# Performance work log

Hardware: AMD Instinct MI355X
Metric: run time of the kernel (lower is better)

## Reference

```python
import jax, jax.numpy as jnp
import numpy as np

GRID_SIZE = 5
SPLINE_ORDER = 3
NUM_BASIS = GRID_SIZE + SPLINE_ORDER  # 8


def make_grid():
    # knots: grid_size + 2*spline_order + 1 = 12 points over extended [-1,1]
    h = 2.0 / GRID_SIZE
    return (jnp.arange(-SPLINE_ORDER, GRID_SIZE + SPLINE_ORDER + 1, dtype=jnp.float32) * h - 1.0)[None, :]  # (1, 12)


def b_splines(x, grid):
    # x: (N, in) -> bases: (N, in, NUM_BASIS) via Cox-de Boor recursion
    x = x[..., None]  # (N, in, 1)
    bases = ((x >= grid[:, :-1]) & (x < grid[:, 1:])).astype(x.dtype)
    for p in range(1, SPLINE_ORDER + 1):
        left = (x - grid[:, : -(p + 1)]) / (grid[:, p:-1] - grid[:, : -(p + 1)])
        right = (grid[:, p + 1:] - x) / (grid[:, p + 1:] - grid[:, 1:-p])
        bases = left * bases[..., :-1] + right * bases[..., 1:]
    return bases


def kan_linear(x, base_w, spline_w, scaler, grid):
    # x: (N, in); base_w: (out, in); spline_w: (out, in, G); scaler: (out, in)
    base = jnp.einsum('ni,oi->no', jax.nn.silu(x), base_w)
    bases = b_splines(x, grid)  # (N, in, G)
    spline = jnp.einsum('nig,oig->no', bases, spline_w * scaler[..., None])
    return base + spline


def setup_inputs() -> dict:
    key = jax.random.key(0)
    ks = jax.random.split(key, 7)
    H, L = 768, 2
    hidden = jax.random.normal(ks[0], (32, 512, H), dtype=jnp.float32)
    s = 0.1
    return {
        'hidden': hidden,
        'base_w1': jax.random.normal(ks[1], (H, H), jnp.float32) * s,
        'spline_w1': jax.random.normal(ks[2], (H, H, NUM_BASIS), jnp.float32) * s,
        'scaler1': jax.random.normal(ks[3], (H, H), jnp.float32) * s + 1.0,
        'base_w2': jax.random.normal(ks[4], (L, H), jnp.float32) * s,
        'spline_w2': jax.random.normal(ks[5], (L, H, NUM_BASIS), jnp.float32) * s,
        'scaler2': jax.random.normal(ks[6], (L, H), jnp.float32) * s + 1.0,
    }


def reference(hidden, base_w1, spline_w1, scaler1, base_w2, spline_w2, scaler2):
    grid = make_grid()
    B, S, H = hidden.shape
    x = hidden.reshape(-1, H)  # (N, H)
    x = kan_linear(x, base_w1, spline_w1, scaler1, grid)
    x = jax.nn.gelu(x, approximate=False)  # torch F.gelu default = erf
    out = kan_linear(x, base_w2, spline_w2, scaler2, grid)  # (N, L)
    return out.reshape(B, S, -1).squeeze(-1) if out.shape[-1] == 1 else out.reshape(B, S, -1)
```

## Files before the change

kernel.cpp:

```cpp
#include <hip/hip_runtime.h>
#include <math.h>

#define NROWS 16384
#define H     768
#define KEXP  6912
#define NCHUNK 108
#define NITER 54

typedef __attribute__((ext_vector_type(8))) short  bhalf8;
typedef __attribute__((ext_vector_type(4))) float  floatx4;
typedef __attribute__((ext_vector_type(4))) unsigned int uintx4;

__device__ __forceinline__ unsigned short f2bf(float f) {
    unsigned int u = __float_as_uint(f);
    u = (u + 0x7FFFu + ((u >> 16) & 1u)) >> 16;
    return (unsigned short)u;
}
__device__ __forceinline__ float bf2f(unsigned short h) {
    return __uint_as_float(((unsigned int)h) << 16);
}
__device__ __forceinline__ unsigned int pack2(unsigned short a, unsigned short b) {
    return (unsigned int)a | ((unsigned int)b << 16);
}
__device__ __forceinline__ float silu_f(float x) {
    return x * __builtin_amdgcn_rcpf(1.0f + __expf(-x));
}

__device__ __forceinline__ float gelu_fast(float x) {
    float x3 = x * x * x;
    float y = fmaf(x3, 0.0356774081f, x * 0.7978845608f);
    float e = __expf(2.0f * y);
    float th = 1.0f - 2.0f * __builtin_amdgcn_rcpf(e + 1.0f);
    return 0.5f * x * (1.0f + th);
}

__device__ __forceinline__ void kan_bases(float x, float* __restrict__ b) {
    const float c6 = 0.166666666667f;
    float u  = fmaf(x, 2.5f, 5.5f);
    float fj = floorf(u);
    float t  = u - fj;
    int  j0  = (int)fj;
    float t2 = t * t, t3 = t2 * t;
    float n0 = t3 * c6;
    float n1 = fmaf(t3, -0.5f, fmaf(t2, 0.5f, fmaf(t, 0.5f, c6)));
    float n2 = fmaf(t3, 0.5f, fmaf(t2, -1.0f, 0.666666666667f));
    float omt = 1.0f - t;
    float n3 = omt * omt * omt * c6;
#pragma unroll
    for (int c = 0; c < 8; ++c) {
        int d = j0 - c;
        float v = (d == 0) ? n0 : 0.0f;
        v = (d == 1) ? n1 : v;
        v = (d == 2) ? n2 : v;
        v = (d == 3) ? n3 : v;
        b[c] = v;
    }
}

__global__ __launch_bounds__(256) void prep_expand(
    const float* __restrict__ x, const float* __restrict__ bw,
    const float* __restrict__ sw, const float* __restrict__ sc,
    unsigned short* __restrict__ wp, unsigned short* __restrict__ F)
{
    const int b = blockIdx.x, t = threadIdx.x;
    if (b < 6144) {
        const int e0 = b * 2048 + t;
#pragma unroll
        for (int j = 0; j < 8; ++j) {
            int e = e0 + j * 256;
            int n = e / 768;
            int i = e - n * 768;
            float xv = x[e];
            unsigned short* out = F + (size_t)n * KEXP;
            __builtin_nontemporal_store(f2bf(silu_f(xv)), out + i);
            float bb[8];
            kan_bases(xv, bb);
            uintx4 pk;
            pk.x = pack2(f2bf(bb[0]), f2bf(bb[1]));
            pk.y = pack2(f2bf(bb[2]), f2bf(bb[3]));
            pk.z = pack2(f2bf(bb[4]), f2bf(bb[5]));
            pk.w = pack2(f2bf(bb[6]), f2bf(bb[7]));
            __builtin_nontemporal_store(pk, (uintx4*)(out + H + (size_t)i * 8));
        }
    } else {
        const int n = b - 6144;
        const float* bwr = bw + (size_t)n * H;
        unsigned short* out = wp + (size_t)n * KEXP;
        if (t < 96) {
            const float4* xp = (const float4*)(bwr + t * 8);
            float4 v0 = xp[0], v1 = xp[1];
            uintx4 pk;
            pk.x = pack2(f2bf(v0.x), f2bf(v0.y));
            pk.y = pack2(f2bf(v0.z), f2bf(v0.w));
            pk.z = pack2(f2bf(v1.x), f2bf(v1.y));
            pk.w = pack2(f2bf(v1.z), f2bf(v1.w));
            __builtin_nontemporal_store(pk, (uintx4*)(out + t * 8));
        }
#pragma unroll
        for (int p = 0; p < 3; ++p) {
            int i = t + p * 256;
            float s = sc[(size_t)n * H + i];
            const float4* swp = (const float4*)(sw + ((size_t)n * H + i) * 8);
            float4 w0 = swp[0], w1 = swp[1];
            uintx4 pk;
            pk.x = pack2(f2bf(w0.x * s), f2bf(w0.y * s));
            pk.y = pack2(f2bf(w0.z * s), f2bf(w0.w * s));
            pk.z = pack2(f2bf(w1.x * s), f2bf(w1.y * s));
            pk.w = pack2(f2bf(w1.z * s), f2bf(w1.w * s));
            __builtin_nontemporal_store(pk, (uintx4*)(out + H + (size_t)i * 8));
        }
    }
}


#define AS1 __attribute__((address_space(1)))
#define AS3 __attribute__((address_space(3)))

#define DSR(D, A, O) asm volatile("ds_read_b128 %0, %1 offset:" #O : "=v"(D) : "v"(A) : "memory")
#define LDA0(O) do{ DSR(fA0[0],avA[0],O); DSR(fA0[1],avA[1],O); DSR(fA0[2],avA[2],O); DSR(fA0[3],avA[3],O); \
                    DSR(fA0[4],avA[4],O); DSR(fA0[5],avA[5],O); DSR(fA0[6],avA[6],O); DSR(fA0[7],avA[7],O); }while(0)
#define LDA1(O) do{ DSR(fA1[0],avA[0],O); DSR(fA1[1],avA[1],O); DSR(fA1[2],avA[2],O); DSR(fA1[3],avA[3],O); \
                    DSR(fA1[4],avA[4],O); DSR(fA1[5],avA[5],O); DSR(fA1[6],avA[6],O); DSR(fA1[7],avA[7],O); }while(0)
#define LDB(O)  do{ DSR(fB[0],avB[0],O); DSR(fB[1],avB[1],O); }while(0)

#define MM0(QN) do{ \
    _Pragma("unroll") \
    for (int kk = 0; kk < 2; ++kk) \
        _Pragma("unroll") \
        for (int im = 0; im < 4; ++im) \
            acc0[QN][im] = __builtin_amdgcn_mfma_f32_16x16x32_bf16( \
                fA0[im*2+kk], fB[kk], acc0[QN][im], 0, 0, 0); \
}while(0)
#define MM1(QN) do{ \
    _Pragma("unroll") \
    for (int kk = 0; kk < 2; ++kk) \
        _Pragma("unroll") \
        for (int im = 0; im < 4; ++im) \
            acc1[QN][im] = __builtin_amdgcn_mfma_f32_16x16x32_bf16( \
                fA1[im*2+kk], fB[kk], acc1[QN][im], 0, 0, 0); \
}while(0)

#define STG_A(BF,HH,KS) do{ \
    __builtin_amdgcn_global_load_lds((const AS1 void*)(pA##HH[0] + (size_t)(KS)*64), \
        (AS3 void*)&sA[BF][HH][wb8], 16, 0, 0); \
    __builtin_amdgcn_global_load_lds((const AS1 void*)(pA##HH[1] + (size_t)(KS)*64), \
        (AS3 void*)&sA[BF][HH][4096 + wb8], 16, 0, 0); \
}while(0)
#define STG_B(BF,QN,KS) \
    __builtin_amdgcn_global_load_lds((const AS1 void*)(pB[QN] + (size_t)(KS)*64), \
        (AS3 void*)&sB[BF][QN][wb8], 16, 0, 0)

#define PH_MID do{ __builtin_amdgcn_s_barrier(); \
    asm volatile("s_waitcnt lgkmcnt(0)" ::: "memory"); \
    __builtin_amdgcn_sched_barrier(0); \
    __builtin_amdgcn_s_setprio(1); }while(0)
#define PH_END do{ __builtin_amdgcn_s_setprio(0); \
    __builtin_amdgcn_sched_barrier(0); \
    __builtin_amdgcn_s_barrier(); }while(0)
#define PH_END_VMN(N) do{ __builtin_amdgcn_s_setprio(0); \
    __builtin_amdgcn_sched_barrier(0); \
    asm volatile("s_waitcnt vmcnt(" #N ")" ::: "memory"); \
    __builtin_amdgcn_s_barrier(); }while(0)

#define EPI_HALF(ACC, QMOFF) do{ \
    float pa[4][4] = {}, pb[4][4] = {}; \
    _Pragma("unroll") \
    for (int qn = 0; qn < 3; ++qn) { \
        const int i = colBase + qn*64 + wc*16 + lm; \
        const float bwa = bw2[i], bwb = bw2[H + i]; \
        const float sca = sc2[i], scb = sc2[H + i]; \
        const float4* q0 = (const float4*)(sw2 + (size_t)i * 8); \
        const float4* q1 = (const float4*)(sw2 + (size_t)(H + i) * 8); \
        const float4 wa0 = q0[0], wa1 = q0[1]; \
        const float4 wb0 = q1[0], wb1 = q1[1]; \
        _Pragma("unroll") \
        for (int im = 0; im < 4; ++im) \
        _Pragma("unroll") \
        for (int rg = 0; rg < 4; ++rg) { \
            float u = gelu_fast(ACC[qn][im][rg]); \
            float f0v = silu_f(u); \
            float bb[8]; \
            kan_bases(u, bb); \
            float t0 = bb[0]*wa0.x + bb[1]*wa0.y + bb[2]*wa0.z + bb[3]*wa0.w \
                     + bb[4]*wa1.x + bb[5]*wa1.y + bb[6]*wa1.z + bb[7]*wa1.w; \
            float t1 = bb[0]*wb0.x + bb[1]*wb0.y + bb[2]*wb0.z + bb[3]*wb0.w \
                     + bb[4]*wb1.x + bb[5]*wb1.y + bb[6]*wb1.z + bb[7]*wb1.w; \
            pa[im][rg] += fmaf(f0v, bwa, sca * t0); \
            pb[im][rg] += fmaf(f0v, bwb, scb * t1); \
        } \
    } \
    _Pragma("unroll") \
    for (int im = 0; im < 4; ++im) \
    _Pragma("unroll") \
    for (int rg = 0; rg < 4; ++rg) { \
        float a0 = pa[im][rg], a1 = pb[im][rg]; \
        _Pragma("unroll") \
        for (int off = 8; off > 0; off >>= 1) { \
            a0 += __shfl_xor(a0, off, 64); \
            a1 += __shfl_xor(a1, off, 64); \
        } \
        if (lm == 0) { \
            const int row = rowBase + (QMOFF) + wr*64 + im*16 + quad*4 + rg; \
            atomicAdd(&outp[(size_t)row * 2 + 0], a0); \
            atomicAdd(&outp[(size_t)row * 2 + 1], a1); \
        } \
    } \
}while(0)

__global__ __launch_bounds__(512, 1) void kan1_fused(
    const unsigned short* __restrict__ F, const unsigned short* __restrict__ wp,
    const float* __restrict__ bw2, const float* __restrict__ sw2,
    const float* __restrict__ sc2, float* __restrict__ outp)
{
    __shared__ __align__(16) unsigned short sA[2][2][8192];
    __shared__ __align__(16) unsigned short sB[2][3][4096];

    const int b = blockIdx.x;
    const int s = b >> 3;
    const int rowT = (b & 7) * 8 + (s >> 2);
    const int colT = s & 3;
    const int rowBase = rowT * 256, colBase = colT * 192;

    const int t = threadIdx.x;
    const int lane = t & 63;
    const int quad = lane >> 4, lm = lane & 15, p7 = lane & 7;
    const int wv = t >> 6, wr = wv & 1, wc = wv >> 1;

    const int rr = t >> 3;
    const int slotx = (t & 7) ^ (rr & 7);
    const int wb8 = (t & 448) * 8;

    const unsigned short* pA0[2]; const unsigned short* pA1[2];
    const unsigned short* pB[3];
#pragma unroll
    for (int p = 0; p < 2; ++p) {
        pA0[p] = F + (size_t)(rowBase +       p*64 + rr) * KEXP + slotx*8;
        pA1[p] = F + (size_t)(rowBase + 128 + p*64 + rr) * KEXP + slotx*8;
    }
#pragma unroll
    for (int q = 0; q < 3; ++q)
        pB[q] = wp + (size_t)(colBase + q*64 + rr) * KEXP + slotx*8;

    unsigned int avA[8], avB[2];
    {
        unsigned int aB = (unsigned int)(size_t)(AS3 unsigned short*)&sA[0][0][0];
        unsigned int bB = (unsigned int)(size_t)(AS3 unsigned short*)&sB[0][0][0];
#pragma unroll
        for (int im = 0; im < 4; ++im)
#pragma unroll
            for (int kk = 0; kk < 2; ++kk)
                avA[im*2+kk] = aB + (unsigned)(((wr*64 + im*16 + lm)*64 + (((kk*4+quad)^p7)*8)) * 2);
#pragma unroll
        for (int kk = 0; kk < 2; ++kk)
            avB[kk] = bB + (unsigned)(((wc*16 + lm)*64 + (((kk*4+quad)^p7)*8)) * 2);
    }

    floatx4 acc0[3][4] = {};
    floatx4 acc1[3][4] = {};
    bhalf8 fA0[8], fA1[8], fB[2];

    STG_A(0,0,0); STG_A(0,1,0); STG_B(0,0,0); STG_B(0,1,0); STG_B(0,2,0);
    STG_A(1,0,1); STG_A(1,1,1); STG_B(1,0,1); STG_B(1,1,1);
    asm volatile("s_waitcnt vmcnt(8)" ::: "memory");
    __builtin_amdgcn_s_barrier();

#pragma unroll 1
    for (int i = 0; i < NITER; ++i) {
        const int k1 = 2*i + 1;
        const int k2 = (2*i + 2 > 107) ? 107 : 2*i + 2;
        const int k3 = (2*i + 3 > 107) ? 107 : 2*i + 3;
        LDA0(0);     LDB(0);     STG_B(1,2,k1);               PH_MID; MM0(0);         PH_END_VMN(10);
        LDA1(16384);             STG_A(0,0,k2);               PH_MID; MM1(0);         PH_END_VMN(10);
        LDB(8192);               STG_A(0,1,k2);               PH_MID; MM1(1); MM0(1); PH_END_VMN(11);
        LDB(16384);              STG_B(0,0,k2); STG_B(0,1,k2);PH_MID; MM0(2); MM1(2); PH_END_VMN(8);
        LDA0(32768); LDB(24576); STG_B(0,2,k2);               PH_MID; MM0(0);         PH_END;
        LDA1(49152);             STG_A(1,0,k3);               PH_MID; MM1(0);         PH_END_VMN(10);
        LDB(32768);              STG_A(1,1,k3);               PH_MID; MM1(1); MM0(1); PH_END_VMN(11);
        LDB(40960);              STG_B(1,0,k3); STG_B(1,1,k3);PH_MID; MM0(2); MM1(2); PH_END_VMN(8);
    }

    EPI_HALF(acc0, 0);
    EPI_HALF(acc1, 128);
}

extern "C" void kernel_launch(void* const* d_in, const int* in_sizes, int n_in,
                              void* d_out, int out_size, void* d_ws, size_t ws_size,
                              hipStream_t stream) {
    const float* hidden = (const float*)d_in[0];
    const float* bw1    = (const float*)d_in[1];
    const float* sw1    = (const float*)d_in[2];
    const float* sc1    = (const float*)d_in[3];
    const float* bw2    = (const float*)d_in[4];
    const float* sw2    = (const float*)d_in[5];
    const float* sc2    = (const float*)d_in[6];
    float* out = (float*)d_out;

    const size_t wp_elems = (size_t)H * KEXP;
    unsigned short* wp = (unsigned short*)d_ws;
    unsigned short* F  = wp + wp_elems;

    hipMemsetAsync(d_out, 0, (size_t)out_size, stream);
    prep_expand<<<6144 + H, 256, 0, stream>>>(hidden, bw1, sw1, sc1, wp, F);
    kan1_fused<<<256, 512, 0, stream>>>(F, wp, bw2, sw2, sc2, out);
}
```

Measured before the change: 310.8 us.

## Evaluate layer-2 cubic B-spline with uniform-knot closed form and LDS weight gather

In the epilogue, the full eight-basis Cox-de Boor evaluation plus two eight-term dot products is replaced by a closed-form uniform cubic B-spline. It computes only the four nonzero basis values from the knot index and fractional position, then gathers matching weights. The layer-2 spline weights, pre-multiplied by their scalers, are staged into shared memory (reusing the A tile buffer) after the main loop. This cuts per-element ALU work in the epilogue, at the cost of an extra full drain, two block barriers, and indexed LDS loads.

Result: slower. 465.2 us (+49.7%).

```diff
diff --git a/kernel.cpp b/kernel.cpp
--- a/kernel.cpp
+++ b/kernel.cpp
@@ -162,31 +162,41 @@
     asm volatile("s_waitcnt vmcnt(" #N ")" ::: "memory"); \
     __builtin_amdgcn_s_barrier(); }while(0)
 
+#define GATH(ND, GEXPR) do{ \
+    int g_ = (GEXPR); \
+    int gc_ = (g_ < 0) ? 0 : ((g_ > 7) ? 7 : g_); \
+    float2 w_ = wt2[((unsigned)gc_ << 10) + (unsigned)iw]; \
+    float ndm_ = (g_ <= 7) ? (ND) : 0.0f; \
+    pa_ = fmaf(ndm_, w_.x, pa_); \
+    pb_ = fmaf(ndm_, w_.y, pb_); \
+}while(0)
+
 #define EPI_HALF(ACC, QMOFF) do{ \
     float pa[4][4] = {}, pb[4][4] = {}; \
     _Pragma("unroll") \
     for (int qn = 0; qn < 3; ++qn) { \
-        const int i = colBase + qn*64 + wc*16 + lm; \
-        const float bwa = bw2[i], bwb = bw2[H + i]; \
-        const float sca = sc2[i], scb = sc2[H + i]; \
-        const float4* q0 = (const float4*)(sw2 + (size_t)i * 8); \
-        const float4* q1 = (const float4*)(sw2 + (size_t)(H + i) * 8); \
-        const float4 wa0 = q0[0], wa1 = q0[1]; \
-        const float4 wb0 = q1[0], wb1 = q1[1]; \
+        const int iw = colBase + qn*64 + wc*16 + lm; \
+        const float bwa = bw2[iw], bwb = bw2[H + iw]; \
         _Pragma("unroll") \
         for (int im = 0; im < 4; ++im) \
         _Pragma("unroll") \
         for (int rg = 0; rg < 4; ++rg) { \
             float u = gelu_fast(ACC[qn][im][rg]); \
             float f0v = silu_f(u); \
-            float bb[8]; \
-            kan_bases(u, bb); \
-            float t0 = bb[0]*wa0.x + bb[1]*wa0.y + bb[2]*wa0.z + bb[3]*wa0.w \
-                     + bb[4]*wa1.x + bb[5]*wa1.y + bb[6]*wa1.z + bb[7]*wa1.w; \
-            float t1 = bb[0]*wb0.x + bb[1]*wb0.y + bb[2]*wb0.z + bb[3]*wb0.w \
-                     + bb[4]*wb1.x + bb[5]*wb1.y + bb[6]*wb1.z + bb[7]*wb1.w; \
-            pa[im][rg] += fmaf(f0v, bwa, sca * t0); \
-            pb[im][rg] += fmaf(f0v, bwb, scb * t1); \
+            float uu = fmaf(u, 2.5f, 5.5f); \
+            float fj = floorf(uu); \
+            float tt = uu - fj; \
+            int j0 = (int)fj; \
+            float tq = tt * tt, tc = tq * tt; \
+            float n0 = tc * 0.166666666667f; \
+            float n1 = fmaf(tc, -0.5f, fmaf(tq, 0.5f, fmaf(tt, 0.5f, 0.166666666667f))); \
+            float n2 = fmaf(tc, 0.5f, fmaf(tq, -1.0f, 0.666666666667f)); \
+            float omt = 1.0f - tt; \
+            float n3 = omt * omt * omt * 0.166666666667f; \
+            float pa_ = 0.f, pb_ = 0.f; \
+            GATH(n0, j0); GATH(n1, j0 - 1); GATH(n2, j0 - 2); GATH(n3, j0 - 3); \
+            pa[im][rg] += fmaf(f0v, bwa, pa_); \
+            pb[im][rg] += fmaf(f0v, bwb, pb_); \
         } \
     } \
     _Pragma("unroll") \
@@ -279,6 +289,24 @@
         LDB(40960);              STG_B(1,0,k3); STG_B(1,1,k3);PH_MID; MM0(2); MM1(2); PH_END_VMN(8);
     }
 
+    asm volatile("s_waitcnt vmcnt(0)" ::: "memory");
+    __syncthreads();
+    {
+        float* wt = (float*)&sA[0][0][0];
+#pragma unroll
+        for (int c = 0; c < 32; ++c) {
+            int lin = t + c * 512;
+            int g   = lin >> 11;
+            int rem = lin & 2047;
+            int iw  = rem >> 1, o = rem & 1;
+            float v = 0.0f;
+            if (iw < H) v = sw2[((size_t)o * H + iw) * 8 + g] * sc2[(size_t)o * H + iw];
+            wt[lin] = v;
+        }
+    }
+    __syncthreads();
+    const float2* wt2 = (const float2*)&sA[0][0][0];
+
     EPI_HALF(acc0, 0);
     EPI_HALF(acc1, 128);
 }
```
